# Kernel optimization log

Hardware: AMD Instinct MI355X
Metric: run time of the kernel (lower is better)

Reference implementation:

```python
import jax, jax.numpy as jnp
import numpy as np

N = 100000  # nodes
E = 320000  # edges
G = 64      # graphs in the batch


def setup_inputs() -> dict:
    key = jax.random.key(0)
    ks = jax.random.split(key, 16)
    inp = {
        "x": jax.random.normal(ks[0], (N, 512), dtype=jnp.float32),
        "edge_index": jax.random.randint(ks[1], (2, E), 0, N, dtype=jnp.int64),
        "batch": jnp.sort(jax.random.randint(ks[2], (N,), 0, G, dtype=jnp.int64)),
    }
    # GCNConv weights (in, out) and biases, Glorot-ish scale
    dims = [(512, 256), (256, 128), (128, 64), (64, 32)]
    for i, (din, dout) in enumerate(dims):
        inp[f"w{i+1}"] = jax.random.normal(ks[3 + i], (din, dout), dtype=jnp.float32) / np.sqrt(din)
        inp[f"b{i+1}"] = jnp.zeros((dout,), dtype=jnp.float32)
    inp["lw1"] = jax.random.normal(ks[8], (32, 16), dtype=jnp.float32) / np.sqrt(32.0)
    inp["lb1"] = jnp.zeros((16,), dtype=jnp.float32)
    inp["lw2"] = jax.random.normal(ks[9], (16, 2), dtype=jnp.float32) / np.sqrt(16.0)
    inp["lb2"] = jnpp = jnp.zeros((2,), dtype=jnp.float32)
    return inp


def _gcn_conv(h_in, w, b, src, dst, norm, n):
    # x' = D^-1/2 (A+I) D^-1/2 (X W) + b   (PyG GCNConv default)
    h = h_in @ w                                  # [N, out]
    msg = h[src] * norm[:, None]                  # gather + scale over edges(+self-loops)
    out = jax.ops.segment_sum(msg, dst, num_segments=n)  # scatter-add
    return out + b


def reference(x, edge_index, batch, w1, b1, w2, b2, w3, b3, w4, b4, lw1, lb1, lw2, lb2):
    n = x.shape[0]
    loop = jnp.arange(n, dtype=edge_index.dtype)
    src = jnp.concatenate([edge_index[0], loop])  # add self-loops
    dst = jnp.concatenate([edge_index[1], loop])
    # symmetric normalization: deg counted at dst (col) including self-loops
    deg = jax.ops.segment_sum(jnp.ones_like(dst, dtype=x.dtype), dst, num_segments=n)
    dinv = jnp.where(deg > 0, 1.0 / jnp.sqrt(deg), 0.0)
    norm = dinv[src] * dinv[dst]                  # [E+N]

    h = jax.nn.relu(_gcn_conv(x, w1, b1, src, dst, norm, n))
    h = jax.nn.relu(_gcn_conv(h, w2, b2, src, dst, norm, n))
    h = jax.nn.relu(_gcn_conv(h, w3, b3, src, dst, norm, n))
    h = _gcn_conv(h, w4, b4, src, dst, norm, n)   # [N, 32]

    # global mean pool over graphs
    sums = jax.ops.segment_sum(h, batch, num_segments=G)
    cnt = jax.ops.segment_sum(jnp.ones((n,), dtype=h.dtype), batch, num_segments=G)
    pooled = sums / jnp.maximum(cnt, 1.0)[:, None]  # [G, 32]

    # dropout p=0.8 is identity in eval mode
    out = jax.nn.relu(pooled @ lw1 + lb1) @ lw2 + lb2  # [G, 2]
    return out
```

## Files before the change

### kernel.cpp

```cpp
#include <hip/hip_runtime.h>
#include <cstdint>
#include <cstddef>


typedef __attribute__((ext_vector_type(8))) short s16x8;
typedef __attribute__((ext_vector_type(4))) float f32x4;

__device__ __forceinline__ short2 split2(float f) {
    union { float f; unsigned u; } c; c.f = f;
    short hi = (short)(c.u >> 16);
    union { unsigned u; float f; } h; h.u = c.u & 0xffff0000u;
    union { float f; unsigned u; } r; r.f = f - h.f;
    short lo = (short)(r.u >> 16);
    return make_short2(hi, lo);
}

__device__ __forceinline__ float bf2f(unsigned short u) {
    union { unsigned v; float f; } c; c.v = ((unsigned)u) << 16; return c.f;
}

__device__ __forceinline__ void gload16(const void* g, void* l) {
    __builtin_amdgcn_global_load_lds(
        (const __attribute__((address_space(1))) unsigned int*)g,
        (__attribute__((address_space(3))) unsigned int*)l, 16, 0, 0);
}


__global__ void k_count(const int* __restrict__ dst, int E, int* __restrict__ cnt) {
    int e = blockIdx.x * blockDim.x + threadIdx.x;
    if (e < E) atomicAdd(&cnt[dst[e]], 1);
}

__global__ void k_scan_sums(const int* __restrict__ cnt, int n, int* __restrict__ bsum) {
    __shared__ int s[256];
    int t = threadIdx.x;
    int base = blockIdx.x * 4096 + t * 16;
    int sum = 0;
#pragma unroll
    for (int j = 0; j < 16; ++j) { int i = base + j; if (i < n) sum += cnt[i]; }
    s[t] = sum;
    __syncthreads();
    for (int off = 128; off > 0; off >>= 1) {
        if (t < off) s[t] += s[t + off];
        __syncthreads();
    }
    if (t == 0) bsum[blockIdx.x] = s[0];
}

__global__ void k_scan_offsets(const int* __restrict__ bsum, int nb,
                               int* __restrict__ boff, int* __restrict__ totalp) {
    int t = threadIdx.x;
    int v = (t < nb) ? bsum[t] : 0;
    int x = v;
    for (int off = 1; off < 64; off <<= 1) {
        int y = __shfl_up(x, off);
        if (t >= off) x += y;
    }
    if (t < nb) boff[t] = x - v;
    if (t == 63) *totalp = x;
}

__global__ void k_scan_final(const int* __restrict__ cnt, int n,
                             const int* __restrict__ boff, int* __restrict__ row_ptr,
                             float* __restrict__ dinv) {
    __shared__ int s[256];
    int t = threadIdx.x;
    int base = blockIdx.x * 4096 + t * 16;
    int v[16]; int sum = 0;
#pragma unroll
    for (int j = 0; j < 16; ++j) { int i = base + j; v[j] = (i < n) ? cnt[i] : 0; sum += v[j]; }
    s[t] = sum;
    __syncthreads();
    for (int off = 1; off < 256; off <<= 1) {
        int y = (t >= off) ? s[t - off] : 0;
        __syncthreads();
        s[t] += y;
        __syncthreads();
    }
    int run = boff[blockIdx.x] + ((t == 0) ? 0 : s[t - 1]);
#pragma unroll
    for (int j = 0; j < 16; ++j) {
        int i = base + j;
        if (i < n) {
            row_ptr[i] = run;
            dinv[i] = rsqrtf((float)(v[j] + 1));
        }
        run += v[j];
    }
}

__global__ void k_fill(const int* __restrict__ src, const int* __restrict__ dst, int E,
                       const int* __restrict__ row_ptr, int* __restrict__ cursor,
                       const float* __restrict__ dinv,
                       int* __restrict__ csr_src, float* __restrict__ csr_norm) {
    int e = blockIdx.x * blockDim.x + threadIdx.x;
    if (e >= E) return;
    int d = dst[e];
    int s = src[e];
    int p = atomicAdd(&cursor[d], 1);
    int slot = row_ptr[d] + p;
    csr_src[slot]  = s;
    csr_norm[slot] = dinv[s] * dinv[d];
}


__global__ void k_split_w_all(const float* __restrict__ w1, const float* __restrict__ w2,
                              const float* __restrict__ w3, const float* __restrict__ w4,
                              unsigned short* __restrict__ w1h, unsigned short* __restrict__ w1l,
                              unsigned short* __restrict__ w2h, unsigned short* __restrict__ w2l,
                              unsigned short* __restrict__ w3h, unsigned short* __restrict__ w3l,
                              unsigned short* __restrict__ w4h, unsigned short* __restrict__ w4l) {
    int idx = blockIdx.x * blockDim.x + threadIdx.x;
    const float* w; unsigned short *th, *tl; int N, ks, loc;
    if (idx < 131072)      { w = w1; th = w1h; tl = w1l; N = 256; ks = 9; loc = idx; }
    else if (idx < 163840) { w = w2; th = w2h; tl = w2l; N = 128; ks = 8; loc = idx - 131072; }
    else if (idx < 172032) { w = w3; th = w3h; tl = w3l; N = 64;  ks = 7; loc = idx - 163840; }
    else if (idx < 174080) { w = w4; th = w4h; tl = w4l; N = 32;  ks = 6; loc = idx - 172032; }
    else return;
    int nn = loc >> ks;
    int k  = loc & ((1 << ks) - 1);
    short2 p = split2(w[(size_t)k * N + nn]);
    th[loc] = (unsigned short)p.x;
    tl[loc] = (unsigned short)p.y;
}


__global__ __launch_bounds__(256)
void k_gemm1(const float* __restrict__ A32,
             const unsigned short* __restrict__ Bth, const unsigned short* __restrict__ Btl,
             unsigned short* __restrict__ Chi, unsigned short* __restrict__ Clo, int M) {
    constexpr int K = 512, KT = 16;
    constexpr int APL = 128 * 64;
    constexpr int BPL = 128 * 64;
    __shared__ char sA[2][2 * APL];
    __shared__ char sB[2][2 * BPL];

    const int tid  = threadIdx.x;
    const int lane = tid & 63;
    const int w    = tid >> 6;
    const int wm   = w & 1;
    const int wn   = w >> 1;
    const int brow = blockIdx.y * 128;
    const int bcol = blockIdx.x * 128;
    const int l15  = lane & 15;
    const int kb   = (lane >> 4) * 16;

    const int arow  = tid >> 1;
    const int ahalf = tid & 1;
    int ag = brow + arow; if (ag > M - 1) ag = M - 1;
    const float* xrow = A32 + (size_t)ag * K + ahalf * 16;
    const int vq = (arow >> 1) & 3;
    const int q0 = ((2 * ahalf) ^ vq) * 16;
    const int q1 = ((2 * ahalf + 1) ^ vq) * 16;

    f32x4 acc[4][4];
#pragma unroll
    for (int i = 0; i < 4; ++i)
#pragma unroll
        for (int j = 0; j < 4; ++j) acc[i][j] = (f32x4){0.f, 0.f, 0.f, 0.f};

    float4 xr[2][4];

    auto X = [&](int t, int p) {
        const float4* q = (const float4*)(xrow + t * 32);
        xr[p][0] = q[0]; xr[p][1] = q[1]; xr[p][2] = q[2]; xr[p][3] = q[3];
    };
    auto WA = [&](char* abuf, int p) {
        float v[16] = {xr[p][0].x, xr[p][0].y, xr[p][0].z, xr[p][0].w,
                       xr[p][1].x, xr[p][1].y, xr[p][1].z, xr[p][1].w,
                       xr[p][2].x, xr[p][2].y, xr[p][2].z, xr[p][2].w,
                       xr[p][3].x, xr[p][3].y, xr[p][3].z, xr[p][3].w};
        s16x8 h0, h1, l0, l1;
#pragma unroll
        for (int j = 0; j < 8; ++j) { short2 q = split2(v[j]);     h0[j] = q.x; l0[j] = q.y; }
#pragma unroll
        for (int j = 0; j < 8; ++j) { short2 q = split2(v[8 + j]); h1[j] = q.x; l1[j] = q.y; }
        *(s16x8*)(abuf + arow * 64 + q0)       = h0;
        *(s16x8*)(abuf + arow * 64 + q1)       = h1;
        *(s16x8*)(abuf + APL + arow * 64 + q0) = l0;
        *(s16x8*)(abuf + APL + arow * 64 + q1) = l1;
    };
    auto SB = [&](char* bbuf, int t) {
#pragma unroll
        for (int u = 0; u < 4; ++u) {
            int id = w + u * 4;
            int hi = (id < 8) ? 1 : 0;
            int s  = hi ? id : id - 8;
            int p  = s * 64 + lane;
            int kq = (p ^ ((p >> 3) & 3)) & 3;
            int col = p >> 2;
            const unsigned short* gs = (hi ? Bth : Btl) + (size_t)(bcol + col) * K + t * 32 + kq * 8;
            gload16(gs, (hi ? bbuf : bbuf + BPL) + s * 1024);
        }
    };
    auto MM = [&](char* abuf, char* bbuf) {
        char* sAl = abuf + APL;
        char* sBl = bbuf + BPL;
        s16x8 fah[4], fam[4];
#pragma unroll
        for (int i = 0; i < 4; ++i) {
            int row = wm * 64 + i * 16 + l15;
            int o = row * 64 + (kb ^ (((row >> 1) & 3) << 4));
            fah[i] = *(const s16x8*)(abuf + o);
            fam[i] = *(const s16x8*)(sAl + o);
        }
#pragma unroll
        for (int j = 0; j < 4; ++j) {
            int col = wn * 64 + j * 16 + l15;
            int o = col * 64 + (kb ^ (((col >> 1) & 3) << 4));
            s16x8 fbh = *(const s16x8*)(bbuf + o);
            s16x8 fbm = *(const s16x8*)(sBl + o);
#pragma unroll
            for (int i = 0; i < 4; ++i) {
                acc[i][j] = __builtin_amdgcn_mfma_f32_16x16x32_bf16(fah[i], fbh, acc[i][j], 0, 0, 0);
                acc[i][j] = __builtin_amdgcn_mfma_f32_16x16x32_bf16(fam[i], fbh, acc[i][j], 0, 0, 0);
                acc[i][j] = __builtin_amdgcn_mfma_f32_16x16x32_bf16(fah[i], fbm, acc[i][j], 0, 0, 0);
            }
        }
    };

    X(0, 0);
    X(1, 1);
    SB(sB[0], 0);
    WA(sA[0], 0);
    __syncthreads();

#pragma unroll
    for (int t = 0; t < KT; ++t) {
        if (t + 2 < KT) X(t + 2, t & 1);
        if (t + 1 < KT) SB(sB[(t + 1) & 1], t + 1);
        MM(sA[t & 1], sB[t & 1]);
        if (t + 1 < KT) WA(sA[(t + 1) & 1], (t + 1) & 1);
        __syncthreads();
    }

#pragma unroll
    for (int i = 0; i < 4; ++i) {
#pragma unroll
        for (int r = 0; r < 4; ++r) {
            int row = brow + wm * 64 + i * 16 + (lane >> 4) * 4 + r;
            if (row >= M) continue;
#pragma unroll
            for (int j = 0; j < 4; ++j) {
                int col = bcol + wn * 64 + j * 16 + l15;
                short2 pq = split2(acc[i][j][r]);
                Chi[(size_t)row * 256 + col] = (unsigned short)pq.x;
                Clo[(size_t)row * 256 + col] = (unsigned short)pq.y;
            }
        }
    }
}


template <int BM, int BN, int GM, int GN, int FM, int FN>
__global__ __launch_bounds__(256)
void k_gemm(const unsigned short* __restrict__ Ah, const unsigned short* __restrict__ Al,
            const unsigned short* __restrict__ Bth, const unsigned short* __restrict__ Btl,
            unsigned short* __restrict__ Chi, unsigned short* __restrict__ Clo,
            int M, int K, int N) {
    static_assert(GM * FM * 16 == BM && GN * FN * 16 == BN && GM * GN == 4, "geom");
    constexpr int ABYTES = BM * 64;
    constexpr int BBYTES = BN * 64;
    constexpr int NSEGA = BM / 16;
    constexpr int NSEGB = BN / 16;
    static_assert((2 * NSEGA) % 4 == 0 && (2 * NSEGB) % 4 == 0, "segs");
    constexpr int BUF = 2 * ABYTES + 2 * BBYTES;
    __shared__ char lds[2 * BUF];

    const int tid  = threadIdx.x;
    const int lane = tid & 63;
    const int w    = tid >> 6;
    const int wm   = w % GM;
    const int wn   = w / GM;
    const int brow = blockIdx.y * BM;
    const int bcol = blockIdx.x * BN;
    const int l15  = lane & 15;
    const int kb   = (lane >> 4) * 16;

    f32x4 acc[FM][FN];
#pragma unroll
    for (int i = 0; i < FM; ++i)
#pragma unroll
        for (int j = 0; j < FN; ++j) acc[i][j] = (f32x4){0.f, 0.f, 0.f, 0.f};

    auto stageA = [&](char* base, int k0) {
#pragma unroll
        for (int u = 0; u < (2 * NSEGA) / 4; ++u) {
            int id = w + u * 4;
            int hi = (id < NSEGA) ? 1 : 0;
            int s  = hi ? id : id - NSEGA;
            int p  = s * 64 + lane;
            int kq = (p ^ ((p >> 3) & 3)) & 3;
            int row = p >> 2;
            const unsigned short* gs = (hi ? Ah : Al) + (size_t)(brow + row) * K + k0 + kq * 8;
            gload16(gs, base + (hi ? 0 : ABYTES) + s * 1024);
        }
    };
    auto stageB = [&](char* base, int k0) {
        char* sBh = base + 2 * ABYTES;
        char* sBl = sBh + BBYTES;
#pragma unroll
        for (int u = 0; u < (2 * NSEGB) / 4; ++u) {
            int id = w + u * 4;
            int hi = (id < NSEGB) ? 1 : 0;
            int s  = hi ? id : id - NSEGB;
            int p  = s * 64 + lane;
            int kq = (p ^ ((p >> 3) & 3)) & 3;
            int col = p >> 2;
            const unsigned short* gs = (hi ? Bth : Btl) + (size_t)(bcol + col) * K + k0 + kq * 8;
            gload16(gs, (hi ? sBh : sBl) + s * 1024);
        }
    };

    char* cur = lds;
    char* nxt = lds + BUF;
    stageB(cur, 0);
    stageA(cur, 0);
    __syncthreads();

    const int KT = K / 32;
    for (int t = 0; t < KT; ++t) {
        const int k1 = (t + 1) * 32;
        if (t + 1 < KT) {
            stageB(nxt, k1);
            stageA(nxt, k1);
        }
        {
            char* sAh = cur;
            char* sAl = cur + ABYTES;
            char* sBh = cur + 2 * ABYTES;
            char* sBl = sBh + BBYTES;
            s16x8 fah[FM], fam[FM];
#pragma unroll
            for (int i = 0; i < FM; ++i) {
                int row = wm * FM * 16 + i * 16 + l15;
                int o = row * 64 + (kb ^ (((row >> 1) & 3) << 4));
                fah[i] = *(const s16x8*)(sAh + o);
                fam[i] = *(const s16x8*)(sAl + o);
            }
#pragma unroll
            for (int j = 0; j < FN; ++j) {
                int col = wn * FN * 16 + j * 16 + l15;
                int o = col * 64 + (kb ^ (((col >> 1) & 3) << 4));
                s16x8 fbh = *(const s16x8*)(sBh + o);
                s16x8 fbm = *(const s16x8*)(sBl + o);
#pragma unroll
                for (int i = 0; i < FM; ++i) {
                    acc[i][j] = __builtin_amdgcn_mfma_f32_16x16x32_bf16(fah[i], fbh, acc[i][j], 0, 0, 0);
                    acc[i][j] = __builtin_amdgcn_mfma_f32_16x16x32_bf16(fam[i], fbh, acc[i][j], 0, 0, 0);
                    acc[i][j] = __builtin_amdgcn_mfma_f32_16x16x32_bf16(fah[i], fbm, acc[i][j], 0, 0, 0);
                }
            }
        }
        __syncthreads();
        char* tmp = cur; cur = nxt; nxt = tmp;
    }

#pragma unroll
    for (int i = 0; i < FM; ++i) {
#pragma unroll
        for (int r = 0; r < 4; ++r) {
            int row = brow + wm * FM * 16 + i * 16 + (lane >> 4) * 4 + r;
            if (row >= M) continue;
#pragma unroll
            for (int j = 0; j < FN; ++j) {
                int col = bcol + wn * FN * 16 + j * 16 + l15;
                short2 pq = split2(acc[i][j][r]);
                Chi[(size_t)row * N + col] = (unsigned short)pq.x;
                Clo[(size_t)row * N + col] = (unsigned short)pq.y;
            }
        }
    }
}


__global__ void k_agg_split(const unsigned short* __restrict__ hhi,
                            const unsigned short* __restrict__ hlo,
                            const int* __restrict__ row_ptr,
                            const int* __restrict__ csr_src, const float* __restrict__ csr_norm,
                            const float* __restrict__ dinv, const float* __restrict__ bias,
                            unsigned short* __restrict__ oh, unsigned short* __restrict__ ol,
                            int n, int f_shift) {
    int idx = blockIdx.x * blockDim.x + threadIdx.x;
    int dout4 = 1 << f_shift;
    int total = n << f_shift;
    if (idx >= total) return;
    int i = idx >> f_shift;
    int f = idx & (dout4 - 1);
    const int drow = dout4 * 4;
    size_t ebase = (size_t)i * drow + f * 4;

    float di = dinv[i];
    float sn = di * di;
    ushort4 sh = *(const ushort4*)(hhi + ebase);
    ushort4 sl = *(const ushort4*)(hlo + ebase);
    float4 acc;
    acc.x = (bf2f(sh.x) + bf2f(sl.x)) * sn;
    acc.y = (bf2f(sh.y) + bf2f(sl.y)) * sn;
    acc.z = (bf2f(sh.z) + bf2f(sl.z)) * sn;
    acc.w = (bf2f(sh.w) + bf2f(sl.w)) * sn;

    int e = row_ptr[i], s1 = row_ptr[i + 1];
    for (; e + 1 < s1; e += 2) {
        int   sa = csr_src[e],      sb = csr_src[e + 1];
        float na = csr_norm[e],     nb = csr_norm[e + 1];
        ushort4 va = *(const ushort4*)(hhi + (size_t)sa * drow + f * 4);
        ushort4 vb = *(const ushort4*)(hhi + (size_t)sb * drow + f * 4);
        acc.x += bf2f(va.x) * na + bf2f(vb.x) * nb;
        acc.y += bf2f(va.y) * na + bf2f(vb.y) * nb;
        acc.z += bf2f(va.z) * na + bf2f(vb.z) * nb;
        acc.w += bf2f(va.w) * na + bf2f(vb.w) * nb;
    }
    if (e < s1) {
        int   s = csr_src[e];
        float nm = csr_norm[e];
        ushort4 v = *(const ushort4*)(hhi + (size_t)s * drow + f * 4);
        acc.x += bf2f(v.x) * nm; acc.y += bf2f(v.y) * nm;
        acc.z += bf2f(v.z) * nm; acc.w += bf2f(v.w) * nm;
    }

    const float4* b4 = (const float4*)bias;
    float4 b = b4[f];
    float4 o;
    o.x = fmaxf(acc.x + b.x, 0.f);
    o.y = fmaxf(acc.y + b.y, 0.f);
    o.z = fmaxf(acc.z + b.z, 0.f);
    o.w = fmaxf(acc.w + b.w, 0.f);

    short2 p0 = split2(o.x), p1 = split2(o.y), p2 = split2(o.z), p3 = split2(o.w);
    *(ushort4*)(oh + ebase) = make_ushort4((unsigned short)p0.x, (unsigned short)p1.x,
                                           (unsigned short)p2.x, (unsigned short)p3.x);
    *(ushort4*)(ol + ebase) = make_ushort4((unsigned short)p0.y, (unsigned short)p1.y,
                                           (unsigned short)p2.y, (unsigned short)p3.y);
}


__global__ void k_agg(const unsigned short* __restrict__ hhi,
                      const unsigned short* __restrict__ hlo,
                      const int* __restrict__ row_ptr,
                      const int* __restrict__ csr_src, const float* __restrict__ csr_norm,
                      const float* __restrict__ dinv, const float* __restrict__ bias,
                      float4* __restrict__ out, int n, int f_shift) {
    int idx = blockIdx.x * blockDim.x + threadIdx.x;
    int dout4 = 1 << f_shift;
    int total = n << f_shift;
    if (idx >= total) return;
    int i = idx >> f_shift;
    int f = idx & (dout4 - 1);
    const int drow = dout4 * 4;
    size_t ebase = (size_t)i * drow + f * 4;

    float di = dinv[i];
    float sn = di * di;
    ushort4 sh = *(const ushort4*)(hhi + ebase);
    ushort4 sl = *(const ushort4*)(hlo + ebase);
    float4 acc;
    acc.x = (bf2f(sh.x) + bf2f(sl.x)) * sn;
    acc.y = (bf2f(sh.y) + bf2f(sl.y)) * sn;
    acc.z = (bf2f(sh.z) + bf2f(sl.z)) * sn;
    acc.w = (bf2f(sh.w) + bf2f(sl.w)) * sn;

    int e = row_ptr[i], s1 = row_ptr[i + 1];
    for (; e + 1 < s1; e += 2) {
        int   sa = csr_src[e],      sb = csr_src[e + 1];
        float na = csr_norm[e],     nb = csr_norm[e + 1];
        ushort4 va = *(const ushort4*)(hhi + (size_t)sa * drow + f * 4);
        ushort4 vb = *(const ushort4*)(hhi + (size_t)sb * drow + f * 4);
        acc.x += bf2f(va.x) * na + bf2f(vb.x) * nb;
        acc.y += bf2f(va.y) * na + bf2f(vb.y) * nb;
        acc.z += bf2f(va.z) * na + bf2f(vb.z) * nb;
        acc.w += bf2f(va.w) * na + bf2f(vb.w) * nb;
    }
    if (e < s1) {
        int   s = csr_src[e];
        float nm = csr_norm[e];
        ushort4 v = *(const ushort4*)(hhi + (size_t)s * drow + f * 4);
        acc.x += bf2f(v.x) * nm; acc.y += bf2f(v.y) * nm;
        acc.z += bf2f(v.z) * nm; acc.w += bf2f(v.w) * nm;
    }

    const float4* b4 = (const float4*)bias;
    float4 b = b4[f];
    float4 o;
    o.x = acc.x + b.x;
    o.y = acc.y + b.y;
    o.z = acc.z + b.z;
    o.w = acc.w + b.w;
    out[(size_t)i * dout4 + f] = o;
}


__global__ void k_pool(const float* __restrict__ h, const int* __restrict__ batch,
                       int n, float* __restrict__ pooled) {
    int g = blockIdx.x;
    int start, end;
    {
        int lo = 0, hi = n;
        while (lo < hi) { int mid = (lo + hi) >> 1; if (batch[mid] < g) lo = mid + 1; else hi = mid; }
        start = lo;
        lo = start; hi = n;
        while (lo < hi) { int mid = (lo + hi) >> 1; if (batch[mid] < g + 1) lo = mid + 1; else hi = mid; }
        end = lo;
    }
    int f = threadIdx.x & 31;
    int sub = threadIdx.x >> 5;
    float s = 0.f;
    for (int i = start + sub; i < end; i += 8) s += h[(size_t)i * 32 + f];
    __shared__ float red[8][32];
    red[sub][f] = s;
    __syncthreads();
    if (sub == 0) {
        float t = 0.f;
#pragma unroll
        for (int k = 0; k < 8; ++k) t += red[k][f];
        int c = end - start;
        pooled[g * 32 + f] = t / (float)(c > 0 ? c : 1);
    }
}


__global__ void k_mlp(const float* __restrict__ pooled, const float* __restrict__ lw1,
                      const float* __restrict__ lb1, const float* __restrict__ lw2,
                      const float* __restrict__ lb2, float* __restrict__ out, int g_count) {
    int g = threadIdx.x;
    if (g >= g_count) return;
    float p[32];
#pragma unroll
    for (int k = 0; k < 32; ++k) p[k] = pooled[g * 32 + k];
    float hmid[16];
#pragma unroll
    for (int j = 0; j < 16; ++j) {
        float s = lb1[j];
#pragma unroll
        for (int k = 0; k < 32; ++k) s += p[k] * lw1[k * 16 + j];
        hmid[j] = fmaxf(s, 0.f);
    }
#pragma unroll
    for (int o = 0; o < 2; ++o) {
        float s = lb2[o];
#pragma unroll
        for (int k = 0; k < 16; ++k) s += hmid[k] * lw2[k * 2 + o];
        out[g * 2 + o] = s;
    }
}


extern "C" void kernel_launch(void* const* d_in, const int* in_sizes, int n_in,
                              void* d_out, int out_size, void* d_ws, size_t ws_size,
                              hipStream_t stream) {
    const float* x     = (const float*)d_in[0];
    const int*   ei    = (const int*)d_in[1];
    const int*   batch = (const int*)d_in[2];
    const float* w1 = (const float*)d_in[3];  const float* b1 = (const float*)d_in[4];
    const float* w2 = (const float*)d_in[5];  const float* b2 = (const float*)d_in[6];
    const float* w3 = (const float*)d_in[7];  const float* b3 = (const float*)d_in[8];
    const float* w4 = (const float*)d_in[9];  const float* b4 = (const float*)d_in[10];
    const float* lw1 = (const float*)d_in[11]; const float* lb1 = (const float*)d_in[12];
    const float* lw2 = (const float*)d_in[13]; const float* lb2 = (const float*)d_in[14];
    float* out = (float*)d_out;

    const int n = in_sizes[0] / 512;
    const int E = in_sizes[1] / 2;
    const int G = 64;

    const int* src = ei;
    const int* dst = ei + E;

    char* ws = (char*)d_ws;
    size_t off = 0;
    auto alloc = [&](size_t bytes) -> void* {
        void* p = ws + off;
        off = (off + bytes + 255) & ~((size_t)255);
        return p;
    };
    unsigned short* ghi  = (unsigned short*)alloc((size_t)n * 256 * 2);
    unsigned short* glo  = (unsigned short*)alloc((size_t)n * 256 * 2);
    unsigned short* pAh  = (unsigned short*)alloc((size_t)n * 256 * 2);
    unsigned short* pAl  = (unsigned short*)alloc((size_t)n * 256 * 2);
    int*   cnt      = (int*)alloc((size_t)n * sizeof(int));
    int*   cursor   = (int*)alloc((size_t)n * sizeof(int));
    int*   row_ptr  = (int*)alloc((size_t)(n + 1) * sizeof(int));
    int*   csr      = (int*)alloc((size_t)E * sizeof(int));
    float* csr_norm = (float*)alloc((size_t)E * sizeof(float));
    float* dinv     = (float*)alloc((size_t)n * sizeof(float));
    float* pooled   = (float*)alloc((size_t)G * 32 * sizeof(float));
    int*   bsum     = (int*)alloc(64 * sizeof(int));
    int*   boff     = (int*)alloc(64 * sizeof(int));
    unsigned short* w1h = (unsigned short*)alloc(256 * 512 * 2);
    unsigned short* w1l = (unsigned short*)alloc(256 * 512 * 2);
    unsigned short* w2h = (unsigned short*)alloc(128 * 256 * 2);
    unsigned short* w2l = (unsigned short*)alloc(128 * 256 * 2);
    unsigned short* w3h = (unsigned short*)alloc(64 * 128 * 2);
    unsigned short* w3l = (unsigned short*)alloc(64 * 128 * 2);
    unsigned short* w4h = (unsigned short*)alloc(32 * 64 * 2);
    unsigned short* w4l = (unsigned short*)alloc(32 * 64 * 2);
    float* bufB = (float*)(pAl + (size_t)n * 64);
    (void)ws_size;

    hipMemsetAsync(cnt, 0, (size_t)n * sizeof(int), stream);
    hipMemsetAsync(cursor, 0, (size_t)n * sizeof(int), stream);

    k_split_w_all<<<(174080 + 255) / 256, 256, 0, stream>>>(
        w1, w2, w3, w4, w1h, w1l, w2h, w2l, w3h, w3l, w4h, w4l);

    const int nscan = (n + 4095) / 4096;
    k_count<<<(E + 255) / 256, 256, 0, stream>>>(dst, E, cnt);
    k_scan_sums   <<<nscan, 256, 0, stream>>>(cnt, n, bsum);
    k_scan_offsets<<<1, 64, 0, stream>>>(bsum, nscan, boff, row_ptr + n);
    k_scan_final  <<<nscan, 256, 0, stream>>>(cnt, n, boff, row_ptr, dinv);
    k_fill<<<(E + 255) / 256, 256, 0, stream>>>(src, dst, E, row_ptr, cursor, dinv, csr, csr_norm);

    const int gy128 = (n + 127) / 128;
    const int gy64  = (n + 63) / 64;

    k_gemm1<<<dim3(2, gy128), 256, 0, stream>>>(x, w1h, w1l, ghi, glo, n);
    k_agg_split<<<((size_t)n * 64 + 255) / 256, 256, 0, stream>>>(
        ghi, glo, row_ptr, csr, csr_norm, dinv, b1, pAh, pAl, n, 6);

    k_gemm<64, 128, 1, 4, 4, 2><<<dim3(1, gy64), 256, 0, stream>>>(
        pAh, pAl, w2h, w2l, ghi, glo, n, 256, 128);
    k_agg_split<<<((size_t)n * 32 + 255) / 256, 256, 0, stream>>>(
        ghi, glo, row_ptr, csr, csr_norm, dinv, b2, pAh, pAl, n, 5);

    k_gemm<64, 64, 1, 4, 4, 1><<<dim3(1, gy64), 256, 0, stream>>>(
        pAh, pAl, w3h, w3l, ghi, glo, n, 128, 64);
    k_agg_split<<<((size_t)n * 16 + 255) / 256, 256, 0, stream>>>(
        ghi, glo, row_ptr, csr, csr_norm, dinv, b3, pAh, pAl, n, 4);

    k_gemm<64, 32, 2, 2, 2, 1><<<dim3(1, gy64), 256, 0, stream>>>(
        pAh, pAl, w4h, w4l, ghi, glo, n, 64, 32);
    k_agg<<<((size_t)n * 8 + 255) / 256, 256, 0, stream>>>(
        ghi, glo, row_ptr, csr, csr_norm, dinv, b4, (float4*)bufB, n, 3);

    k_pool<<<G, 256, 0, stream>>>(bufB, batch, n, pooled);
    k_mlp<<<1, 64, 0, stream>>>(pooled, lw1, lb1, lw2, lb2, out, G);
}
```

Before: 477.3 us.

## Load fp32 A tiles directly to LDS and split to bf16 at fragment read

```diff
diff --git a/kernel.cpp b/kernel.cpp
--- a/kernel.cpp
+++ b/kernel.cpp
@@ -130,10 +130,10 @@
              const unsigned short* __restrict__ Bth, const unsigned short* __restrict__ Btl,
              unsigned short* __restrict__ Chi, unsigned short* __restrict__ Clo, int M) {
     constexpr int K = 512, KT = 16;
-    constexpr int APL = 128 * 64;
+    constexpr int ASZ = 128 * 128;
     constexpr int BPL = 128 * 64;
-    __shared__ char sA[2][2 * APL];
-    __shared__ char sB[2][2 * BPL];
+    __shared__ char sAf[ASZ];
+    __shared__ char sB[2 * BPL];
 
     const int tid  = threadIdx.x;
     const int lane = tid & 63;
@@ -145,42 +145,25 @@
     const int l15  = lane & 15;
     const int kb   = (lane >> 4) * 16;
 
-    const int arow  = tid >> 1;
-    const int ahalf = tid & 1;
-    int ag = brow + arow; if (ag > M - 1) ag = M - 1;
-    const float* xrow = A32 + (size_t)ag * K + ahalf * 16;
-    const int vq = (arow >> 1) & 3;
-    const int q0 = ((2 * ahalf) ^ vq) * 16;
-    const int q1 = ((2 * ahalf + 1) ^ vq) * 16;
-
     f32x4 acc[4][4];
 #pragma unroll
     for (int i = 0; i < 4; ++i)
 #pragma unroll
         for (int j = 0; j < 4; ++j) acc[i][j] = (f32x4){0.f, 0.f, 0.f, 0.f};
 
-    float4 xr[2][4];
-
-    auto X = [&](int t, int p) {
-        const float4* q = (const float4*)(xrow + t * 32);
-        xr[p][0] = q[0]; xr[p][1] = q[1]; xr[p][2] = q[2]; xr[p][3] = q[3];
+    auto SA = [&](int t) {
+#pragma unroll
+        for (int u = 0; u < 4; ++u) {
+            int c   = u * 256 + tid;
+            int row = c >> 3;
+            int cl  = c & 7;
+            int cs  = cl ^ (row & 7);
+            int rg  = brow + row; if (rg > M - 1) rg = M - 1;
+            const float* gs = A32 + (size_t)rg * K + t * 32 + cs * 4;
+            gload16(gs, sAf + (u * 256 + w * 64) * 16);
+        }
     };
-    auto WA = [&](char* abuf, int p) {
-        float v[16] = {xr[p][0].x, xr[p][0].y, xr[p][0].z, xr[p][0].w,
-                       xr[p][1].x, xr[p][1].y, xr[p][1].z, xr[p][1].w,
-                       xr[p][2].x, xr[p][2].y, xr[p][2].z, xr[p][2].w,
-                       xr[p][3].x, xr[p][3].y, xr[p][3].z, xr[p][3].w};
-        s16x8 h0, h1, l0, l1;
-#pragma unroll
-        for (int j = 0; j < 8; ++j) { short2 q = split2(v[j]);     h0[j] = q.x; l0[j] = q.y; }
-#pragma unroll
-        for (int j = 0; j < 8; ++j) { short2 q = split2(v[8 + j]); h1[j] = q.x; l1[j] = q.y; }
-        *(s16x8*)(abuf + arow * 64 + q0)       = h0;
-        *(s16x8*)(abuf + arow * 64 + q1)       = h1;
-        *(s16x8*)(abuf + APL + arow * 64 + q0) = l0;
-        *(s16x8*)(abuf + APL + arow * 64 + q1) = l1;
-    };
-    auto SB = [&](char* bbuf, int t) {
+    auto SB = [&](int t) {
 #pragma unroll
         for (int u = 0; u < 4; ++u) {
             int id = w + u * 4;
@@ -190,25 +173,31 @@
             int kq = (p ^ ((p >> 3) & 3)) & 3;
             int col = p >> 2;
             const unsigned short* gs = (hi ? Bth : Btl) + (size_t)(bcol + col) * K + t * 32 + kq * 8;
-            gload16(gs, (hi ? bbuf : bbuf + BPL) + s * 1024);
+            gload16(gs, (hi ? sB : sB + BPL) + s * 1024);
         }
     };
-    auto MM = [&](char* abuf, char* bbuf) {
-        char* sAl = abuf + APL;
-        char* sBl = bbuf + BPL;
+    auto MM = [&]() {
+        char* sBl = sB + BPL;
         s16x8 fah[4], fam[4];
 #pragma unroll
         for (int i = 0; i < 4; ++i) {
             int row = wm * 64 + i * 16 + l15;
-            int o = row * 64 + (kb ^ (((row >> 1) & 3) << 4));
-            fah[i] = *(const s16x8*)(abuf + o);
-            fam[i] = *(const s16x8*)(sAl + o);
+            int r7  = row & 7;
+            int c0  = ((lane >> 4) * 2) ^ r7;
+            int c1  = ((lane >> 4) * 2 + 1) ^ r7;
+            float4 v0 = *(const float4*)(sAf + row * 128 + c0 * 16);
+            float4 v1 = *(const float4*)(sAf + row * 128 + c1 * 16);
+            float v[8] = {v0.x, v0.y, v0.z, v0.w, v1.x, v1.y, v1.z, v1.w};
+            s16x8 h, l;
+#pragma unroll
+            for (int jj = 0; jj < 8; ++jj) { short2 q = split2(v[jj]); h[jj] = q.x; l[jj] = q.y; }
+            fah[i] = h; fam[i] = l;
         }
 #pragma unroll
         for (int j = 0; j < 4; ++j) {
             int col = wn * 64 + j * 16 + l15;
             int o = col * 64 + (kb ^ (((col >> 1) & 3) << 4));
-            s16x8 fbh = *(const s16x8*)(bbuf + o);
+            s16x8 fbh = *(const s16x8*)(sB + o);
             s16x8 fbm = *(const s16x8*)(sBl + o);
 #pragma unroll
             for (int i = 0; i < 4; ++i) {
@@ -219,18 +208,11 @@
         }
     };
 
-    X(0, 0);
-    X(1, 1);
-    SB(sB[0], 0);
-    WA(sA[0], 0);
-    __syncthreads();
-
-#pragma unroll
     for (int t = 0; t < KT; ++t) {
-        if (t + 2 < KT) X(t + 2, t & 1);
-        if (t + 1 < KT) SB(sB[(t + 1) & 1], t + 1);
-        MM(sA[t & 1], sB[t & 1]);
-        if (t + 1 < KT) WA(sA[(t + 1) & 1], (t + 1) & 1);
+        SA(t);
+        SB(t);
+        __syncthreads();
+        MM();
         __syncthreads();
     }
 
```

New measurement: 491.9 us. 1.03x slower.
